# Performance work log

Hardware: AMD Instinct MI355X
Metric: run time of the kernel (lower is better)

## Reference

```python
import jax, jax.numpy as jnp
import numpy as np

N0, N1, N2 = 100000, 50000, 25000
E0, E1 = 400000, 200000
H1, D1 = 4, 64   # layer0: 4 heads x 64
H2, D2 = 1, 64   # layer1: 1 head  x 64
SLOPE = 0.2      # DGL GATConv leaky_relu negative_slope


def gat_conv(h_src, h_dst, src, dst, W, attn_l, attn_r, bias, n_dst, heads, d):
    # linear projection (shared between src and dst, as in DGL GATConv)
    f_src = (h_src @ W).reshape(-1, heads, d)   # (N_src, H, D)
    f_dst = (h_dst @ W).reshape(-1, heads, d)   # (N_dst, H, D)
    el = jnp.einsum('nhd,hd->nh', f_src, attn_l)  # (N_src, H)
    er = jnp.einsum('nhd,hd->nh', f_dst, attn_r)  # (N_dst, H)
    e = jax.nn.leaky_relu(el[src] + er[dst], SLOPE)  # (E, H)
    # edge-softmax over incoming edges of each dst node (numerically stable)
    m = jax.ops.segment_max(e, dst, num_segments=n_dst)      # (N_dst, H)
    ee = jnp.exp(e - m[dst])
    s = jax.ops.segment_sum(ee, dst, num_segments=n_dst)
    alpha = ee / s[dst]                                      # (E, H)
    msg = f_src[src] * alpha[:, :, None]                     # (E, H, D)
    out = jax.ops.segment_sum(msg, dst, num_segments=n_dst)  # (N_dst, H, D)
    return out + bias.reshape(1, heads, d)


def setup_inputs() -> dict:
    key = jax.random.key(0)
    ks = jax.random.split(key, 12)
    return {
        'x': jax.random.normal(ks[0], (N0, 256), jnp.float32),
        'e0_src': jax.random.randint(ks[1], (E0,), 0, N0, jnp.int32),
        'e0_dst': jax.random.randint(ks[2], (E0,), 0, N1, jnp.int32),
        'e1_src': jax.random.randint(ks[3], (E1,), 0, N1, jnp.int32),
        'e1_dst': jax.random.randint(ks[4], (E1,), 0, N2, jnp.int32),
        'W1': jax.random.normal(ks[5], (256, H1 * D1), jnp.float32) * 0.06,
        'al1': jax.random.normal(ks[6], (H1, D1), jnp.float32) * 0.1,
        'ar1': jax.random.normal(ks[7], (H1, D1), jnp.float32) * 0.1,
        'b1': jnp.zeros((H1 * D1,), jnp.float32),
        'W2': jax.random.normal(ks[8], (H1 * D1, H2 * D2), jnp.float32) * 0.06,
        'al2': jax.random.normal(ks[9], (H2, D2), jnp.float32) * 0.1,
        'ar2': jax.random.normal(ks[10], (H2, D2), jnp.float32) * 0.1,
        'b2': jnp.zeros((H2 * D2,), jnp.float32),
    }


def reference(x, e0_src, e0_dst, e1_src, e1_dst,
              W1, al1, ar1, b1, W2, al2, ar2, b2):
    # layer 0: block 100k src -> 50k dst; dst nodes are a prefix of src nodes
    h = gat_conv(x, x[:N1], e0_src, e0_dst, W1, al1, ar1, b1, N1, H1, D1)
    h = jax.nn.relu(h).reshape(N1, H1 * D1)   # activation + flatten(1); dropout is identity at eval
    # layer 1 (final): single head, no activation, flatten
    h = gat_conv(h, h[:N2], e1_src, e1_dst, W2, al2, ar2, b2, N2, H2, D2)
    return h.reshape(N2, H2 * D2)
```

## Files before the change

### kernel.cpp

```cpp
#include <hip/hip_runtime.h>
#include <cstddef>
#include <cstdint>

constexpr int cN0 = 100000, cN1 = 50000, cN2 = 25000;
constexpr int cE0 = 400000, cE1 = 200000;
constexpr float SLOPE = 0.2f;

typedef short short8  __attribute__((ext_vector_type(8)));
typedef short short4v __attribute__((ext_vector_type(4)));
typedef float f32x4   __attribute__((ext_vector_type(4)));

__device__ __forceinline__ unsigned short f2bf(float x) {
    union { float f; uint32_t u; } c; c.f = x;
    uint32_t u = c.u + 0x7FFFu + ((c.u >> 16) & 1u);
    return (unsigned short)(u >> 16);
}
__device__ __forceinline__ float bf2f(uint32_t u) {
    union { uint32_t u; float f; } c; c.u = u << 16; return c.f;
}
__device__ __forceinline__ float lrelu(float x) { return x >= 0.f ? x : SLOPE * x; }

__device__ __forceinline__ uint32_t cvtpk(float lo, float hi) {
    uint32_t r;
    asm("v_cvt_pk_bf16_f32 %0, %1, %2" : "=v"(r) : "v"(lo), "v"(hi));
    return r;
}

__device__ __forceinline__ void gload_lds16(const void* g, void* l) {
    __builtin_amdgcn_global_load_lds(
        (const __attribute__((address_space(1))) unsigned int*)g,
        (__attribute__((address_space(3))) unsigned int*)l, 16, 0, 0);
}


__global__ void hist2_kernel(const int* __restrict__ d0, const int* __restrict__ d1,
                             int* __restrict__ cnt0, int* __restrict__ cnt1) {
    int i = blockIdx.x * blockDim.x + threadIdx.x;
    if (i < cE0) atomicAdd(&cnt0[d0[i]], 1);
    int j = i - cE0;
    if (j >= 0 && j < cE1) atomicAdd(&cnt1[d1[j]], 1);
}

__global__ __launch_bounds__(256) void chunk_sum2_kernel(const int* __restrict__ cnt0, int n0,
                                                         const int* __restrict__ cnt1, int n1,
                                                         int* __restrict__ bsum0, int* __restrict__ bsum1,
                                                         int nblk1) {
    const int* cnt = blockIdx.y ? cnt1 : cnt0;
    int n = blockIdx.y ? n1 : n0;
    int* bsum = blockIdx.y ? bsum1 : bsum0;
    if (blockIdx.y && (int)blockIdx.x >= nblk1) return;
    int i = blockIdx.x * 256 + threadIdx.x;
    int v = (i < n) ? cnt[i] : 0;
    #pragma unroll
    for (int o = 32; o; o >>= 1) v += __shfl_xor(v, o);
    __shared__ int ws[4];
    if ((threadIdx.x & 63) == 0) ws[threadIdx.x >> 6] = v;
    __syncthreads();
    if (threadIdx.x == 0) bsum[blockIdx.x] = ws[0] + ws[1] + ws[2] + ws[3];
}

__device__ __forceinline__ int block_exscan(int v, int& total) {
    int lane = threadIdx.x & 63, w = threadIdx.x >> 6;
    int x = v;
    #pragma unroll
    for (int o = 1; o < 64; o <<= 1) { int t = __shfl_up(x, o); if (lane >= o) x += t; }
    __shared__ int ws[4];
    if (lane == 63) ws[w] = x;
    __syncthreads();
    int add = 0;
    #pragma unroll
    for (int i = 0; i < 4; ++i) if (i < w) add += ws[i];
    total = ws[0] + ws[1] + ws[2] + ws[3];
    return add + x - v;
}

__global__ __launch_bounds__(256) void top_scan2_kernel(const int* __restrict__ bsum0, int nblk0,
                                                        const int* __restrict__ bsum1, int nblk1,
                                                        int* __restrict__ boff0, int* __restrict__ boff1,
                                                        int* __restrict__ tot0, int* __restrict__ tot1) {
    int i = threadIdx.x;
    int tot;
    int v = (i < nblk0) ? bsum0[i] : 0;
    int e = block_exscan(v, tot);
    if (i < nblk0) boff0[i] = e;
    if (i == 0) *tot0 = tot;
    __syncthreads();
    v = (i < nblk1) ? bsum1[i] : 0;
    e = block_exscan(v, tot);
    if (i < nblk1) boff1[i] = e;
    if (i == 0) *tot1 = tot;
}

__global__ __launch_bounds__(256) void chunk_scan2_kernel(const int* __restrict__ cnt0, int n0,
                                                          const int* __restrict__ cnt1, int n1,
                                                          const int* __restrict__ boff0, const int* __restrict__ boff1,
                                                          int* __restrict__ offs0, int* __restrict__ cursor0,
                                                          int* __restrict__ offs1, int* __restrict__ cursor1,
                                                          int nblk1) {
    const int* cnt = blockIdx.y ? cnt1 : cnt0;
    const int* boff = blockIdx.y ? boff1 : boff0;
    int* offs = blockIdx.y ? offs1 : offs0;
    int* cursor = blockIdx.y ? cursor1 : cursor0;
    int n = blockIdx.y ? n1 : n0;
    if (blockIdx.y && (int)blockIdx.x >= nblk1) return;
    int i = blockIdx.x * 256 + threadIdx.x;
    int v = (i < n) ? cnt[i] : 0;
    int tot; int e = block_exscan(v, tot) + boff[blockIdx.x];
    if (i < n) { offs[i] = e; cursor[i] = e; }
}

__global__ void scatter2_kernel(const int* __restrict__ s0, const int* __restrict__ d0,
                                const int* __restrict__ s1, const int* __restrict__ d1,
                                int* __restrict__ cursor0, int* __restrict__ srcidx0,
                                int* __restrict__ cursor1, int* __restrict__ srcidx1) {
    int i = blockIdx.x * blockDim.x + threadIdx.x;
    if (i < cE0) { int p = atomicAdd(&cursor0[d0[i]], 1); srcidx0[p] = s0[i]; }
    int j = i - cE0;
    if (j >= 0 && j < cE1) { int p = atomicAdd(&cursor1[d1[j]], 1); srcidx1[p] = s1[j]; }
}

__global__ __launch_bounds__(256) void bf16_transpose2_kernel(const float* __restrict__ W1,
                                                              const float* __restrict__ W2,
                                                              short* __restrict__ bt1,
                                                              short* __restrict__ bt2) {
    int i = blockIdx.x * 256 + threadIdx.x;
    if (i < 256 * 256) {
        int k = i >> 8, n = i & 255;
        bt1[(size_t)n * 256 + k] = (short)f2bf(W1[i]);
    } else {
        int j = i - 256 * 256;
        if (j < 256 * 64) {
            int k = j >> 6, n = j & 63;
            bt2[(size_t)n * 256 + k] = (short)f2bf(W2[j]);
        }
    }
}

__global__ __launch_bounds__(512, 4) void gemm0_deep(
    const float* __restrict__ A, const short* __restrict__ BT,
    unsigned short* __restrict__ C,
    const float* __restrict__ al, const float* __restrict__ ar,
    float* __restrict__ el, float* __restrict__ er,
    int M, int erN)
{
    constexpr int T = 8;
    constexpr int nh = 4;
    __shared__ float Asm[2][128 * 32];
    __shared__ short Bsm[2][256 * 32];

    const int tid = threadIdx.x;
    const int w = tid >> 6;
    const int lane = tid & 63;
    const int ln = lane & 15;
    const int kg = lane >> 4;
    const int wr = w >> 2;
    const int wc = w & 3;
    const int m0 = blockIdx.x * 128;

    f32x4 acc[4][4];
    #pragma unroll
    for (int mi = 0; mi < 4; ++mi)
        #pragma unroll
        for (int ni = 0; ni < 4; ++ni)
            #pragma unroll
            for (int j = 0; j < 4; ++j) acc[mi][ni][j] = 0.f;

    auto stageA = [&](int k0, int b) {
        #pragma unroll
        for (int q = 0; q < 2; ++q) {
            int ci = w + q * 8;
            int r = ci * 8 + (lane >> 3);
            int cl = (lane & 7) ^ (r & 7);
            int gr = m0 + r; if (gr >= M) gr = M - 1;
            gload_lds16(&A[(size_t)gr * 256 + k0 + cl * 4], &Asm[b][ci * 256]);
        }
    };
    auto stageB = [&](int k0, int b) {
        #pragma unroll
        for (int q = 0; q < 2; ++q) {
            int ci = w + q * 8;
            int r = ci * 16 + (lane >> 2);
            int cl = (lane & 3) ^ ((r >> 1) & 3);
            gload_lds16(&BT[(size_t)r * 256 + k0 + cl * 8], &Bsm[b][ci * 512]);
        }
    };

    stageA(0, 0); stageB(0, 0);
    __syncthreads();

    const int swa = ln & 7;
    const int p0base = 2 * kg;
    const int pb = kg ^ ((ln >> 1) & 3);

    int cur = 0;
    #pragma unroll
    for (int t = 0; t < T; ++t) {
        if (t + 1 < T) { stageA((t + 1) * 32, cur ^ 1); stageB((t + 1) * 32, cur ^ 1); }

        short8 af[4];
        {
            int pA = p0base ^ swa;
            #pragma unroll
            for (int mi = 0; mi < 4; ++mi) {
                int r = wr * 64 + mi * 16 + ln;
                const f32x4 q0 = *(const f32x4*)&Asm[cur][r * 32 + pA * 4];
                const f32x4 q1 = *(const f32x4*)&Asm[cur][r * 32 + (pA ^ 1) * 4];
                union { uint32_t u[4]; short8 s; } cv;
                cv.u[0] = cvtpk(q0[0], q0[1]);
                cv.u[1] = cvtpk(q0[2], q0[3]);
                cv.u[2] = cvtpk(q1[0], q1[1]);
                cv.u[3] = cvtpk(q1[2], q1[3]);
                af[mi] = cv.s;
            }
        }
        #pragma unroll
        for (int ni = 0; ni < 4; ++ni) {
            int rB = wc * 64 + ni * 16 + ln;
            short8 bf = *(const short8*)&Bsm[cur][rB * 32 + pb * 8];
            #pragma unroll
            for (int mi = 0; mi < 4; ++mi)
                acc[mi][ni] = __builtin_amdgcn_mfma_f32_16x16x32_bf16(af[mi], bf, acc[mi][ni], 0, 0, 0);
        }
        __syncthreads();
        cur ^= 1;
    }

    const int h = wc;
    float alv[4], arv[4];
    #pragma unroll
    for (int ni = 0; ni < 4; ++ni) {
        alv[ni] = al[h * 64 + ni * 16 + ln];
        arv[ni] = ar[h * 64 + ni * 16 + ln];
    }
    #pragma unroll
    for (int mi = 0; mi < 4; ++mi) {
        float pl[4] = {0, 0, 0, 0}, pr[4] = {0, 0, 0, 0};
        #pragma unroll
        for (int ni = 0; ni < 4; ++ni)
            #pragma unroll
            for (int j = 0; j < 4; ++j) {
                float v = acc[mi][ni][j];
                pl[j] += v * alv[ni];
                pr[j] += v * arv[ni];
            }
        #pragma unroll
        for (int j = 0; j < 4; ++j)
            #pragma unroll
            for (int o = 1; o < 16; o <<= 1) {
                pl[j] += __shfl_xor(pl[j], o);
                pr[j] += __shfl_xor(pr[j], o);
            }
        #pragma unroll
        for (int j = 0; j < 4; ++j) {
            int row = m0 + wr * 64 + mi * 16 + kg * 4 + j;
            if (row < M) {
                #pragma unroll
                for (int ni = 0; ni < 4; ++ni)
                    C[(size_t)row * 256 + wc * 64 + ni * 16 + ln] = f2bf(acc[mi][ni][j]);
                if (ln == 0) {
                    el[row * nh + h] = pl[j];
                    if (row < erN) er[row * nh + h] = pr[j];
                }
            }
        }
    }
}

template<int BM, int BN, int WR, int WC>
__global__ __launch_bounds__(256) void gemm_bf16_fused(
    const unsigned short* __restrict__ A, const short* __restrict__ BT,
    unsigned short* __restrict__ C,
    const float* __restrict__ al, const float* __restrict__ ar,
    float* __restrict__ el, float* __restrict__ er,
    int M, int K, int nh, int erN)
{
    constexpr int BK = 32;
    constexpr int PITCH = BK + 8;
    constexpr int MI = BM / WR / 16;
    constexpr int NI = BN / WC / 16;
    constexpr int AITB = BM * 4 / 256;
    constexpr int BIT  = BN * 4 / 256;

    __shared__ short As[BM * PITCH];
    __shared__ short Bs[BN * PITCH];

    const int tid = threadIdx.x;
    const int w = tid >> 6;
    const int lane = tid & 63;
    const int ln = lane & 15;
    const int kg = lane >> 4;
    const int wr = w / WC;
    const int wc = w % WC;
    const int m0 = blockIdx.x * BM;
    const int n0 = blockIdx.y * BN;
    const int N = nh * 64;

    f32x4 acc[MI][NI];
    #pragma unroll
    for (int mi = 0; mi < MI; ++mi)
        #pragma unroll
        for (int ni = 0; ni < NI; ++ni)
            #pragma unroll
            for (int j = 0; j < 4; ++j) acc[mi][ni][j] = 0.f;

    short8 aregb[AITB];
    short8 breg[BIT];

    auto loadA = [&](int k0) {
        #pragma unroll
        for (int p = 0; p < AITB; ++p) {
            int slot = tid + p * 256;
            int r = slot >> 2;
            int kq = (slot & 3) * 8;
            int gr = m0 + r;
            short8 v = {};
            if (gr < M) v = *(const short8*)&A[(size_t)gr * K + k0 + kq];
            aregb[p] = v;
        }
    };
    auto loadB = [&](int k0) {
        #pragma unroll
        for (int p = 0; p < BIT; ++p) {
            int slot = tid + p * 256;
            int r = slot >> 2;
            int kq = (slot & 3) * 8;
            breg[p] = *(const short8*)&BT[(size_t)(n0 + r) * K + k0 + kq];
        }
    };
    auto writeLDS = [&]() {
        #pragma unroll
        for (int p = 0; p < AITB; ++p) {
            int slot = tid + p * 256;
            int r = slot >> 2;
            int kq = (slot & 3) * 8;
            *(short8*)&As[r * PITCH + kq] = aregb[p];
        }
        #pragma unroll
        for (int p = 0; p < BIT; ++p) {
            int slot = tid + p * 256;
            int r = slot >> 2;
            int kq = (slot & 3) * 8;
            *(short8*)&Bs[r * PITCH + kq] = breg[p];
        }
    };

    loadA(0); loadB(0);
    const int T = K / BK;
    for (int t = 0; t < T; ++t) {
        writeLDS();
        __syncthreads();
        if (t + 1 < T) { loadA((t + 1) * BK); loadB((t + 1) * BK); }
        short8 af[MI], bf[NI];
        #pragma unroll
        for (int mi = 0; mi < MI; ++mi)
            af[mi] = *(const short8*)&As[(wr * MI * 16 + mi * 16 + ln) * PITCH + kg * 8];
        #pragma unroll
        for (int ni = 0; ni < NI; ++ni)
            bf[ni] = *(const short8*)&Bs[(wc * NI * 16 + ni * 16 + ln) * PITCH + kg * 8];
        #pragma unroll
        for (int mi = 0; mi < MI; ++mi)
            #pragma unroll
            for (int ni = 0; ni < NI; ++ni)
                acc[mi][ni] = __builtin_amdgcn_mfma_f32_16x16x32_bf16(af[mi], bf[ni], acc[mi][ni], 0, 0, 0);
        __syncthreads();
    }

    const int h = (n0 + wc * NI * 16) >> 6;
    float alv[NI], arv[NI];
    #pragma unroll
    for (int ni = 0; ni < NI; ++ni) {
        alv[ni] = al[h * 64 + ni * 16 + ln];
        arv[ni] = ar[h * 64 + ni * 16 + ln];
    }
    #pragma unroll
    for (int mi = 0; mi < MI; ++mi) {
        float pl[4] = {0, 0, 0, 0}, pr[4] = {0, 0, 0, 0};
        #pragma unroll
        for (int ni = 0; ni < NI; ++ni)
            #pragma unroll
            for (int j = 0; j < 4; ++j) {
                float v = acc[mi][ni][j];
                pl[j] += v * alv[ni];
                pr[j] += v * arv[ni];
            }
        #pragma unroll
        for (int j = 0; j < 4; ++j)
            #pragma unroll
            for (int o = 1; o < 16; o <<= 1) {
                pl[j] += __shfl_xor(pl[j], o);
                pr[j] += __shfl_xor(pr[j], o);
            }
        #pragma unroll
        for (int j = 0; j < 4; ++j) {
            int row = m0 + wr * MI * 16 + mi * 16 + kg * 4 + j;
            if (row < M) {
                #pragma unroll
                for (int ni = 0; ni < NI; ++ni)
                    C[(size_t)row * N + n0 + wc * NI * 16 + ni * 16 + ln] = f2bf(acc[mi][ni][j]);
                if (ln == 0) {
                    el[row * nh + h] = pl[j];
                    if (row < erN) er[row * nh + h] = pr[j];
                }
            }
        }
    }
}


__global__ __launch_bounds__(256) void agg0_kernel(const int* __restrict__ offs,
                                                   const int* __restrict__ srcidx,
                                                   const float* __restrict__ el,
                                                   const float* __restrict__ er,
                                                   const unsigned short* __restrict__ fb,
                                                   const float* __restrict__ bias,
                                                   unsigned short* __restrict__ h1b) {
    int w = threadIdx.x >> 6, lane = threadIdx.x & 63;
    int n = blockIdx.x * 4 + w;
    if (n >= cN1) return;
    int beg = offs[n], end = offs[n + 1];

    int h4 = lane & 3, sub = lane >> 2;
    float erA = er[n * 4 + h4];
    float m = -1e30f, s = 0.f;
    for (int i = beg + sub; i < end; i += 16) {
        int sv = srcidx[i];
        float e = lrelu(el[sv * 4 + h4] + erA);
        if (e > m) { s = s * __expf(m - e) + 1.f; m = e; }
        else s += __expf(e - m);
    }
    #pragma unroll
    for (int o = 4; o < 64; o <<= 1) {
        float m2 = __shfl_xor(m, o), s2 = __shfl_xor(s, o);
        float M = fmaxf(m, m2);
        s = s * __expf(m - M) + s2 * __expf(m2 - M);
        m = M;
    }
    float inv = (s > 0.f) ? 1.f / s : 0.f;

    int q = lane >> 4, lcol = lane & 15;
    int hB = lcol >> 2;
    float mB = __shfl(m, hB);
    float invB = __shfl(inv, hB);
    float erB = __shfl(erA, hB);

    float a[16] = {};
    for (int i = beg + q; i < end; i += 4) {
        int sv = srcidx[i];
        float e = lrelu(el[sv * 4 + hB] + erB);
        float p = __expf(e - mB) * invB;
        const uint4* rp = (const uint4*)&fb[(size_t)sv * 256 + lcol * 16];
        uint4 v0 = rp[0];
        uint4 v1 = rp[1];
        a[0]  = fmaf(bf2f(v0.x & 0xffffu), p, a[0]);
        a[1]  = fmaf(bf2f(v0.x >> 16),     p, a[1]);
        a[2]  = fmaf(bf2f(v0.y & 0xffffu), p, a[2]);
        a[3]  = fmaf(bf2f(v0.y >> 16),     p, a[3]);
        a[4]  = fmaf(bf2f(v0.z & 0xffffu), p, a[4]);
        a[5]  = fmaf(bf2f(v0.z >> 16),     p, a[5]);
        a[6]  = fmaf(bf2f(v0.w & 0xffffu), p, a[6]);
        a[7]  = fmaf(bf2f(v0.w >> 16),     p, a[7]);
        a[8]  = fmaf(bf2f(v1.x & 0xffffu), p, a[8]);
        a[9]  = fmaf(bf2f(v1.x >> 16),     p, a[9]);
        a[10] = fmaf(bf2f(v1.y & 0xffffu), p, a[10]);
        a[11] = fmaf(bf2f(v1.y >> 16),     p, a[11]);
        a[12] = fmaf(bf2f(v1.z & 0xffffu), p, a[12]);
        a[13] = fmaf(bf2f(v1.z >> 16),     p, a[13]);
        a[14] = fmaf(bf2f(v1.w & 0xffffu), p, a[14]);
        a[15] = fmaf(bf2f(v1.w >> 16),     p, a[15]);
    }
    #pragma unroll
    for (int j = 0; j < 16; ++j) {
        a[j] += __shfl_xor(a[j], 16);
        a[j] += __shfl_xor(a[j], 32);
    }
    if (q == 0) {
        short8 r0, r1;
        #pragma unroll
        for (int j = 0; j < 8; ++j) {
            float o = a[j] + bias[lcol * 16 + j];
            r0[j] = (short)f2bf(o > 0.f ? o : 0.f);
        }
        #pragma unroll
        for (int j = 0; j < 8; ++j) {
            float o = a[8 + j] + bias[lcol * 16 + 8 + j];
            r1[j] = (short)f2bf(o > 0.f ? o : 0.f);
        }
        *(short8*)&h1b[(size_t)n * 256 + lcol * 16] = r0;
        *(short8*)&h1b[(size_t)n * 256 + lcol * 16 + 8] = r1;
    }
}

__global__ __launch_bounds__(256) void agg1_kernel(const int* __restrict__ offs,
                                                   const int* __restrict__ srcidx,
                                                   const float* __restrict__ el,
                                                   const float* __restrict__ er,
                                                   const unsigned short* __restrict__ f2b,
                                                   const float* __restrict__ bias,
                                                   float* __restrict__ out) {
    int w = threadIdx.x >> 6, lane = threadIdx.x & 63;
    int n = blockIdx.x * 4 + w;
    if (n >= cN2) return;
    int beg = offs[n], end = offs[n + 1];
    float ern = er[n];

    float m = -1e30f, s = 0.f;
    for (int i = beg + lane; i < end; i += 64) {
        float e = lrelu(el[srcidx[i]] + ern);
        if (e > m) { s = s * __expf(m - e) + 1.f; m = e; }
        else s += __expf(e - m);
    }
    #pragma unroll
    for (int o = 1; o < 64; o <<= 1) {
        float m2 = __shfl_xor(m, o), s2 = __shfl_xor(s, o);
        float M = fmaxf(m, m2);
        s = s * __expf(m - M) + s2 * __expf(m2 - M);
        m = M;
    }
    float inv = (s > 0.f) ? 1.f / s : 0.f;

    int q = lane >> 3, lcol = lane & 7;
    float a[8] = {};
    for (int i = beg + q; i < end; i += 8) {
        int sv = srcidx[i];
        float e = lrelu(el[sv] + ern);
        float p = __expf(e - m) * inv;
        uint4 v = *(const uint4*)&f2b[(size_t)sv * 64 + lcol * 8];
        a[0] = fmaf(bf2f(v.x & 0xffffu), p, a[0]);
        a[1] = fmaf(bf2f(v.x >> 16),     p, a[1]);
        a[2] = fmaf(bf2f(v.y & 0xffffu), p, a[2]);
        a[3] = fmaf(bf2f(v.y >> 16),     p, a[3]);
        a[4] = fmaf(bf2f(v.z & 0xffffu), p, a[4]);
        a[5] = fmaf(bf2f(v.z >> 16),     p, a[5]);
        a[6] = fmaf(bf2f(v.w & 0xffffu), p, a[6]);
        a[7] = fmaf(bf2f(v.w >> 16),     p, a[7]);
    }
    #pragma unroll
    for (int j = 0; j < 8; ++j) {
        a[j] += __shfl_xor(a[j], 8);
        a[j] += __shfl_xor(a[j], 16);
        a[j] += __shfl_xor(a[j], 32);
    }
    if (q == 0) {
        float4 o0, o1;
        o0.x = a[0] + bias[lcol * 8 + 0];
        o0.y = a[1] + bias[lcol * 8 + 1];
        o0.z = a[2] + bias[lcol * 8 + 2];
        o0.w = a[3] + bias[lcol * 8 + 3];
        o1.x = a[4] + bias[lcol * 8 + 4];
        o1.y = a[5] + bias[lcol * 8 + 5];
        o1.z = a[6] + bias[lcol * 8 + 6];
        o1.w = a[7] + bias[lcol * 8 + 7];
        *(float4*)&out[(size_t)n * 64 + lcol * 8] = o0;
        *(float4*)&out[(size_t)n * 64 + lcol * 8 + 4] = o1;
    }
}


extern "C" void kernel_launch(void* const* d_in, const int* in_sizes, int n_in,
                              void* d_out, int out_size, void* d_ws, size_t ws_size,
                              hipStream_t stream) {
    const float* x      = (const float*)d_in[0];
    const int*   e0_src = (const int*)d_in[1];
    const int*   e0_dst = (const int*)d_in[2];
    const int*   e1_src = (const int*)d_in[3];
    const int*   e1_dst = (const int*)d_in[4];
    const float* W1     = (const float*)d_in[5];
    const float* al1    = (const float*)d_in[6];
    const float* ar1    = (const float*)d_in[7];
    const float* b1     = (const float*)d_in[8];
    const float* W2     = (const float*)d_in[9];
    const float* al2    = (const float*)d_in[10];
    const float* ar2    = (const float*)d_in[11];
    const float* b2     = (const float*)d_in[12];
    float* out = (float*)d_out;

    char* ws = (char*)d_ws;
    size_t off = 0;
    auto alloc = [&](size_t bytes) -> void* {
        void* p = ws + off;
        off = (off + bytes + 255) & ~(size_t)255;
        return p;
    };
    unsigned short* fb  = (unsigned short*)alloc((size_t)cN0 * 256 * 2);
    unsigned short* h1b = (unsigned short*)alloc((size_t)cN1 * 256 * 2);
    unsigned short* f2b = (unsigned short*)alloc((size_t)cN1 * 64 * 2);
    float* el0  = (float*)alloc((size_t)cN0 * 4 * 4);
    float* er0  = (float*)alloc((size_t)cN1 * 4 * 4);
    float* el2  = (float*)alloc((size_t)cN1 * 4);
    float* er2  = (float*)alloc((size_t)cN2 * 4);
    short* bt1  = (short*)alloc((size_t)256 * 256 * 2);
    short* bt2  = (short*)alloc((size_t)64 * 256 * 2);
    int* cntB    = (int*)alloc((size_t)(cN1 + cN2) * 4);
    int* cnt0    = cntB;
    int* cnt1    = cntB + cN1;
    int* offs0   = (int*)alloc((size_t)(cN1 + 1) * 4);
    int* cursor0 = (int*)alloc((size_t)cN1 * 4);
    int* srcidx0 = (int*)alloc((size_t)cE0 * 4);
    int* offs1   = (int*)alloc((size_t)(cN2 + 1) * 4);
    int* cursor1 = (int*)alloc((size_t)cN2 * 4);
    int* srcidx1 = (int*)alloc((size_t)cE1 * 4);
    int* bsum0   = (int*)alloc(256 * 4);
    int* boff0   = (int*)alloc(256 * 4);
    int* bsum1   = (int*)alloc(256 * 4);
    int* boff1   = (int*)alloc(256 * 4);
    (void)ws_size; (void)n_in; (void)in_sizes; (void)out_size;

    const int nblk0 = (cN1 + 255) / 256;
    const int nblk1 = (cN2 + 255) / 256;

    hipMemsetAsync(cntB, 0, (size_t)(cN1 + cN2) * 4, stream);
    hist2_kernel<<<(cE0 + cE1 + 255) / 256, 256, 0, stream>>>(e0_dst, e1_dst, cnt0, cnt1);
    chunk_sum2_kernel<<<dim3(nblk0, 2), 256, 0, stream>>>(cnt0, cN1, cnt1, cN2, bsum0, bsum1, nblk1);
    top_scan2_kernel<<<1, 256, 0, stream>>>(bsum0, nblk0, bsum1, nblk1, boff0, boff1,
                                            offs0 + cN1, offs1 + cN2);
    chunk_scan2_kernel<<<dim3(nblk0, 2), 256, 0, stream>>>(cnt0, cN1, cnt1, cN2, boff0, boff1,
                                                           offs0, cursor0, offs1, cursor1, nblk1);
    scatter2_kernel<<<(cE0 + cE1 + 255) / 256, 256, 0, stream>>>(e0_src, e0_dst, e1_src, e1_dst,
                                                                 cursor0, srcidx0, cursor1, srcidx1);
    bf16_transpose2_kernel<<<(256 * 256 + 256 * 64 + 255) / 256, 256, 0, stream>>>(W1, W2, bt1, bt2);

    gemm0_deep<<<(cN0 + 127) / 128, 512, 0, stream>>>(x, bt1, fb, al1, ar1, el0, er0, cN0, cN1);
    agg0_kernel<<<(cN1 + 3) / 4, 256, 0, stream>>>(offs0, srcidx0, el0, er0, fb, b1, h1b);

    gemm_bf16_fused<128, 64, 4, 1><<<dim3((cN1 + 127) / 128, 1), 256, 0, stream>>>(
        h1b, bt2, f2b, al2, ar2, el2, er2, cN1, 256, 1, cN2);
    agg1_kernel<<<(cN2 + 3) / 4, 256, 0, stream>>>(offs1, srcidx1, el2, er2, f2b, b2, out);
}
```

Baseline: 181.7 us.

## Fuse layer-1 projection GEMM into layer-0 aggregation kernel

Fuses the layer-0 aggregation with the layer-1 linear projection and attention-logit computation. Each 1024-thread block aggregates 16 destination nodes into LDS, then 4 waves run MFMA against W2 staged in LDS to produce f2b, el2 and er2. This removes the h1b intermediate write/read and one kernel launch. In exchange every block reloads the full 32KB W2 tile into LDS, and the large blocks with a sync barrier may reduce occupancy and latency hiding for the irregular gather.

After: 188.2 us. +3.6%, slower.

```diff
diff --git a/kernel.cpp b/kernel.cpp
--- a/kernel.cpp
+++ b/kernel.cpp
@@ -7,7 +7,6 @@
 constexpr float SLOPE = 0.2f;
 
 typedef short short8  __attribute__((ext_vector_type(8)));
-typedef short short4v __attribute__((ext_vector_type(4)));
 typedef float f32x4   __attribute__((ext_vector_type(4)));
 
 __device__ __forceinline__ unsigned short f2bf(float x) {
@@ -266,157 +265,33 @@
     }
 }
 
-template<int BM, int BN, int WR, int WC>
-__global__ __launch_bounds__(256) void gemm_bf16_fused(
-    const unsigned short* __restrict__ A, const short* __restrict__ BT,
-    unsigned short* __restrict__ C,
-    const float* __restrict__ al, const float* __restrict__ ar,
-    float* __restrict__ el, float* __restrict__ er,
-    int M, int K, int nh, int erN)
+__global__ __launch_bounds__(1024) void agg0_fused(
+    const int* __restrict__ offs, const int* __restrict__ srcidx,
+    const float* __restrict__ el, const float* __restrict__ er,
+    const unsigned short* __restrict__ fb, const float* __restrict__ bias,
+    const short* __restrict__ bt2,
+    const float* __restrict__ al2, const float* __restrict__ ar2,
+    unsigned short* __restrict__ f2b, float* __restrict__ el2, float* __restrict__ er2)
 {
-    constexpr int BK = 32;
-    constexpr int PITCH = BK + 8;
-    constexpr int MI = BM / WR / 16;
-    constexpr int NI = BN / WC / 16;
-    constexpr int AITB = BM * 4 / 256;
-    constexpr int BIT  = BN * 4 / 256;
-
-    __shared__ short As[BM * PITCH];
-    __shared__ short Bs[BN * PITCH];
+    constexpr int PITCH = 264;
+    __shared__ short Bs2[64 * 256];
+    __shared__ short h1s[16 * PITCH];
+    __shared__ float partE[4][16];
+    __shared__ float partR[4][16];
 
     const int tid = threadIdx.x;
     const int w = tid >> 6;
     const int lane = tid & 63;
-    const int ln = lane & 15;
-    const int kg = lane >> 4;
-    const int wr = w / WC;
-    const int wc = w % WC;
-    const int m0 = blockIdx.x * BM;
-    const int n0 = blockIdx.y * BN;
-    const int N = nh * 64;
-
-    f32x4 acc[MI][NI];
-    #pragma unroll
-    for (int mi = 0; mi < MI; ++mi)
-        #pragma unroll
-        for (int ni = 0; ni < NI; ++ni)
-            #pragma unroll
-            for (int j = 0; j < 4; ++j) acc[mi][ni][j] = 0.f;
-
-    short8 aregb[AITB];
-    short8 breg[BIT];
-
-    auto loadA = [&](int k0) {
-        #pragma unroll
-        for (int p = 0; p < AITB; ++p) {
-            int slot = tid + p * 256;
-            int r = slot >> 2;
-            int kq = (slot & 3) * 8;
-            int gr = m0 + r;
-            short8 v = {};
-            if (gr < M) v = *(const short8*)&A[(size_t)gr * K + k0 + kq];
-            aregb[p] = v;
-        }
-    };
-    auto loadB = [&](int k0) {
-        #pragma unroll
-        for (int p = 0; p < BIT; ++p) {
-            int slot = tid + p * 256;
-            int r = slot >> 2;
-            int kq = (slot & 3) * 8;
-            breg[p] = *(const short8*)&BT[(size_t)(n0 + r) * K + k0 + kq];
-        }
-    };
-    auto writeLDS = [&]() {
-        #pragma unroll
-        for (int p = 0; p < AITB; ++p) {
-            int slot = tid + p * 256;
-            int r = slot >> 2;
-            int kq = (slot & 3) * 8;
-            *(short8*)&As[r * PITCH + kq] = aregb[p];
-        }
-        #pragma unroll
-        for (int p = 0; p < BIT; ++p) {
-            int slot = tid + p * 256;
-            int r = slot >> 2;
-            int kq = (slot & 3) * 8;
-            *(short8*)&Bs[r * PITCH + kq] = breg[p];
-        }
-    };
-
-    loadA(0); loadB(0);
-    const int T = K / BK;
-    for (int t = 0; t < T; ++t) {
-        writeLDS();
-        __syncthreads();
-        if (t + 1 < T) { loadA((t + 1) * BK); loadB((t + 1) * BK); }
-        short8 af[MI], bf[NI];
-        #pragma unroll
-        for (int mi = 0; mi < MI; ++mi)
-            af[mi] = *(const short8*)&As[(wr * MI * 16 + mi * 16 + ln) * PITCH + kg * 8];
-        #pragma unroll
-        for (int ni = 0; ni < NI; ++ni)
-            bf[ni] = *(const short8*)&Bs[(wc * NI * 16 + ni * 16 + ln) * PITCH + kg * 8];
-        #pragma unroll
-        for (int mi = 0; mi < MI; ++mi)
-            #pragma unroll
-            for (int ni = 0; ni < NI; ++ni)
-                acc[mi][ni] = __builtin_amdgcn_mfma_f32_16x16x32_bf16(af[mi], bf[ni], acc[mi][ni], 0, 0, 0);
-        __syncthreads();
-    }
-
-    const int h = (n0 + wc * NI * 16) >> 6;
-    float alv[NI], arv[NI];
-    #pragma unroll
-    for (int ni = 0; ni < NI; ++ni) {
-        alv[ni] = al[h * 64 + ni * 16 + ln];
-        arv[ni] = ar[h * 64 + ni * 16 + ln];
-    }
-    #pragma unroll
-    for (int mi = 0; mi < MI; ++mi) {
-        float pl[4] = {0, 0, 0, 0}, pr[4] = {0, 0, 0, 0};
-        #pragma unroll
-        for (int ni = 0; ni < NI; ++ni)
-            #pragma unroll
-            for (int j = 0; j < 4; ++j) {
-                float v = acc[mi][ni][j];
-                pl[j] += v * alv[ni];
-                pr[j] += v * arv[ni];
-            }
-        #pragma unroll
-        for (int j = 0; j < 4; ++j)
-            #pragma unroll
-            for (int o = 1; o < 16; o <<= 1) {
-                pl[j] += __shfl_xor(pl[j], o);
-                pr[j] += __shfl_xor(pr[j], o);
-            }
-        #pragma unroll
-        for (int j = 0; j < 4; ++j) {
-            int row = m0 + wr * MI * 16 + mi * 16 + kg * 4 + j;
-            if (row < M) {
-                #pragma unroll
-                for (int ni = 0; ni < NI; ++ni)
-                    C[(size_t)row * N + n0 + wc * NI * 16 + ni * 16 + ln] = f2bf(acc[mi][ni][j]);
-                if (ln == 0) {
-                    el[row * nh + h] = pl[j];
-                    if (row < erN) er[row * nh + h] = pr[j];
-                }
-            }
-        }
-    }
-}
-
-
-__global__ __launch_bounds__(256) void agg0_kernel(const int* __restrict__ offs,
-                                                   const int* __restrict__ srcidx,
-                                                   const float* __restrict__ el,
-                                                   const float* __restrict__ er,
-                                                   const unsigned short* __restrict__ fb,
-                                                   const float* __restrict__ bias,
-                                                   unsigned short* __restrict__ h1b) {
-    int w = threadIdx.x >> 6, lane = threadIdx.x & 63;
-    int n = blockIdx.x * 4 + w;
-    if (n >= cN1) return;
+    const int n = blockIdx.x * 16 + w;
+
+    #pragma unroll
+    for (int i = 0; i < 2; ++i) {
+        int seg = 2 * (i * 16 + w);
+        int r = seg + (lane >> 5);
+        int c = (lane & 31) ^ (r & 7);
+        gload_lds16(&bt2[(size_t)r * 256 + c * 8], &Bs2[(size_t)seg * 256]);
+    }
+
     int beg = offs[n], end = offs[n + 1];
 
     int h4 = lane & 3, sub = lane >> 2;
@@ -473,20 +348,66 @@
         a[j] += __shfl_xor(a[j], 16);
         a[j] += __shfl_xor(a[j], 32);
     }
-    if (q == 0) {
+
+    if (lane < 16) {
+        float4 b0 = *(const float4*)&bias[lane * 16 + 0];
+        float4 b1 = *(const float4*)&bias[lane * 16 + 4];
+        float4 b2 = *(const float4*)&bias[lane * 16 + 8];
+        float4 b3 = *(const float4*)&bias[lane * 16 + 12];
+        float bb[16] = { b0.x, b0.y, b0.z, b0.w, b1.x, b1.y, b1.z, b1.w,
+                         b2.x, b2.y, b2.z, b2.w, b3.x, b3.y, b3.z, b3.w };
         short8 r0, r1;
         #pragma unroll
         for (int j = 0; j < 8; ++j) {
-            float o = a[j] + bias[lcol * 16 + j];
+            float o = a[j] + bb[j];
             r0[j] = (short)f2bf(o > 0.f ? o : 0.f);
         }
         #pragma unroll
         for (int j = 0; j < 8; ++j) {
-            float o = a[8 + j] + bias[lcol * 16 + 8 + j];
+            float o = a[8 + j] + bb[8 + j];
             r1[j] = (short)f2bf(o > 0.f ? o : 0.f);
         }
-        *(short8*)&h1b[(size_t)n * 256 + lcol * 16] = r0;
-        *(short8*)&h1b[(size_t)n * 256 + lcol * 16 + 8] = r1;
+        *(short8*)&h1s[w * PITCH + lane * 16] = r0;
+        *(short8*)&h1s[w * PITCH + lane * 16 + 8] = r1;
+    }
+    __syncthreads();
+
+    if (w < 4) {
+        const int ln = lane & 15, kg = lane >> 4;
+        const int cc = w * 16 + ln;
+        f32x4 acc2;
+        #pragma unroll
+        for (int j = 0; j < 4; ++j) acc2[j] = 0.f;
+        #pragma unroll
+        for (int kt = 0; kt < 8; ++kt) {
+            short8 af = *(const short8*)&h1s[ln * PITCH + kt * 32 + kg * 8];
+            short8 bf = *(const short8*)&Bs2[cc * 256 + ((kt * 4 + kg) ^ (cc & 7)) * 8];
+            acc2 = __builtin_amdgcn_mfma_f32_16x16x32_bf16(af, bf, acc2, 0, 0, 0);
+        }
+        float alc = al2[cc], arc = ar2[cc];
+        #pragma unroll
+        for (int j = 0; j < 4; ++j) {
+            int node = kg * 4 + j;
+            float v = acc2[j];
+            f2b[((size_t)(blockIdx.x * 16 + node)) * 64 + cc] = f2bf(v);
+            float pe = v * alc, pr = v * arc;
+            #pragma unroll
+            for (int o = 1; o < 16; o <<= 1) {
+                pe += __shfl_xor(pe, o);
+                pr += __shfl_xor(pr, o);
+            }
+            if (ln == 0) { partE[w][node] = pe; partR[w][node] = pr; }
+        }
+    }
+    __syncthreads();
+    if (tid < 16) {
+        int gn = blockIdx.x * 16 + tid;
+        float e = partE[0][tid] + partE[1][tid] + partE[2][tid] + partE[3][tid];
+        el2[gn] = e;
+        if (gn < cN2) {
+            float r = partR[0][tid] + partR[1][tid] + partR[2][tid] + partR[3][tid];
+            er2[gn] = r;
+        }
     }
 }
 
@@ -582,7 +503,6 @@
         return p;
     };
     unsigned short* fb  = (unsigned short*)alloc((size_t)cN0 * 256 * 2);
-    unsigned short* h1b = (unsigned short*)alloc((size_t)cN1 * 256 * 2);
     unsigned short* f2b = (unsigned short*)alloc((size_t)cN1 * 64 * 2);
     float* el0  = (float*)alloc((size_t)cN0 * 4 * 4);
     float* er0  = (float*)alloc((size_t)cN1 * 4 * 4);
@@ -620,9 +540,9 @@
     bf16_transpose2_kernel<<<(256 * 256 + 256 * 64 + 255) / 256, 256, 0, stream>>>(W1, W2, bt1, bt2);
 
     gemm0_deep<<<(cN0 + 127) / 128, 512, 0, stream>>>(x, bt1, fb, al1, ar1, el0, er0, cN0, cN1);
-    agg0_kernel<<<(cN1 + 3) / 4, 256, 0, stream>>>(offs0, srcidx0, el0, er0, fb, b1, h1b);
-
-    gemm_bf16_fused<128, 64, 4, 1><<<dim3((cN1 + 127) / 128, 1), 256, 0, stream>>>(
-        h1b, bt2, f2b, al2, ar2, el2, er2, cN1, 256, 1, cN2);
+
+    agg0_fused<<<cN1 / 16, 1024, 0, stream>>>(offs0, srcidx0, el0, er0, fb, b1,
+                                              bt2, al2, ar2, f2b, el2, er2);
+
     agg1_kernel<<<(cN2 + 3) / 4, 256, 0, stream>>>(offs1, srcidx1, el2, er2, f2b, b2, out);
 }
```
